# Kernel tuning notes

Measured on AMD Instinct MI355X. Metric: run time of the kernel, lower is better.

The kernel has to match this reference:

```python
import jax, jax.numpy as jnp
import numpy as np

B, C, H, W = 4, 64, 64, 64

def setup_inputs() -> dict:
    key = jax.random.key(0)
    ks = jax.random.split(key, 7)
    s = 1.0 / np.sqrt(C)
    return {
        "x": jax.random.normal(ks[0], (B, C, H, W), dtype=jnp.float32),
        "Wq": jax.random.normal(ks[1], (C, C), dtype=jnp.float32) * s,
        "bq": jax.random.normal(ks[2], (C,), dtype=jnp.float32) * s,
        "Wk": jax.random.normal(ks[3], (C, C), dtype=jnp.float32) * s,
        "bk": jax.random.normal(ks[4], (C,), dtype=jnp.float32) * s,
        "Wv": jax.random.normal(ks[5], (C, C), dtype=jnp.float32) * s,
        "bv": jax.random.normal(ks[6], (C,), dtype=jnp.float32) * s,
    }

def reference(x, Wq, bq, Wk, bk, Wv, bv):
    b, c, h, w = x.shape
    n = h * w
    xf = x.reshape(b, c, n)                                   # (B,C,N)
    # 1x1 convs == per-pixel linear maps over channels
    q = jnp.einsum('oc,bcn->bon', Wq, xf) + bq[None, :, None]  # (B,C,N)
    k = jnp.einsum('oc,bcn->bon', Wk, xf) + bk[None, :, None]  # (B,C,N)
    v = jnp.einsum('oc,bcn->bon', Wv, xf) + bv[None, :, None]  # (B,C,N)
    # energy = Q^T K : (B,N,N); note: no 1/sqrt(C) scaling in the original
    energy = jnp.einsum('bcn,bcm->bnm', q, k)
    attention = jax.nn.softmax(energy, axis=-1)
    # out = V @ attention^T : out[:, :, i] = sum_j V[:, :, j] * attention[i, j]
    out = jnp.einsum('bcm,bnm->bcn', v, attention)
    return out.reshape(b, c, h, w)
```

## Files before the change

### kernel.cpp

```cpp
#include <hip/hip_runtime.h>
#include <math.h>

#define T_N 4096
#define T_C 64
#define T_B 4
#define NSLICE 8
#define TILES_PER_SLICE (64 / NSLICE)

typedef __attribute__((ext_vector_type(8))) _Float16 f16x8;
typedef __attribute__((ext_vector_type(4))) _Float16 f16x4;
typedef __attribute__((ext_vector_type(4))) float f32x4;

__device__ inline unsigned short f2h(float f) {
    union { _Float16 h; unsigned short s; } u; u.h = (_Float16)f; return u.s;
}
__device__ inline float h2f(unsigned short s) {
    union { unsigned short s; _Float16 h; } u; u.s = s; return (float)u.h;
}

__global__ __launch_bounds__(256) void qkv_kernel(
    const float* __restrict__ x,
    const float* __restrict__ Wq, const float* __restrict__ bq,
    const float* __restrict__ Wk, const float* __restrict__ bk,
    const float* __restrict__ Wv, const float* __restrict__ bv,
    unsigned short* __restrict__ qt, unsigned short* __restrict__ kt,
    unsigned short* __restrict__ vb)
{
    __shared__ __align__(16) unsigned short xsh[32 * 72];
    __shared__ __align__(16) unsigned short xsl[32 * 72];
    __shared__ __align__(16) unsigned short wf[3][64 * 72];

    const int tid = threadIdx.x;
    const int n0  = blockIdx.x * 32;
    const int b   = blockIdx.y;
    const float* xb = x + (size_t)b * T_C * T_N;

    const float* Ws[3] = {Wq, Wk, Wv};
    #pragma unroll
    for (int p = 0; p < 3; ++p) {
        for (int i = tid; i < 1024; i += 256) {
            const int o = i >> 4, c4 = (i & 15) * 4;
            const float4 w4 = ((const float4*)Ws[p])[i];
            f16x4 wh;
            wh[0] = (_Float16)w4.x; wh[1] = (_Float16)w4.y;
            wh[2] = (_Float16)w4.z; wh[3] = (_Float16)w4.w;
            *(f16x4*)&wf[p][o * 72 + c4] = wh;
        }
    }
    for (int i = tid; i < 512; i += 256) {
        const int c = i >> 3, nj4 = (i & 7) * 4;
        const float4 xv = *(const float4*)&xb[c * T_N + n0 + nj4];
        const float xa[4] = {xv.x, xv.y, xv.z, xv.w};
        #pragma unroll
        for (int j = 0; j < 4; ++j) {
            const unsigned short h = f2h(xa[j]);
            xsh[(nj4 + j) * 72 + c] = h;
            xsl[(nj4 + j) * 72 + c] = f2h(xa[j] - h2f(h));
        }
    }
    __syncthreads();

    const int wv_  = tid >> 6;
    const int lane = tid & 63;
    const int quad = lane >> 4;
    const int col  = lane & 15;
    const int pst  = (wv_ & 1) * 16;
    const int oh   = (wv_ >> 1) * 2;
    const size_t bN = (size_t)b * T_N;

    f16x8 xh[2], xl[2];
    #pragma unroll
    for (int s = 0; s < 2; ++s) {
        xh[s] = *(const f16x8*)&xsh[(pst + col) * 72 + s * 32 + quad * 8];
        xl[s] = *(const f16x8*)&xsl[(pst + col) * 72 + s * 32 + quad * 8];
    }
    __syncthreads();

    const float* biases[3] = {bq, bk, bv};
    for (int p = 0; p < 3; ++p) {
        #pragma unroll
        for (int oo = 0; oo < 2; ++oo) {
            const int osub = oh + oo;
            f32x4 acc = (f32x4){0.f, 0.f, 0.f, 0.f};
            #pragma unroll
            for (int s = 0; s < 2; ++s) {
                const f16x8 wfr =
                    *(const f16x8*)&wf[p][(osub * 16 + col) * 72 + s * 32 + quad * 8];
                acc = __builtin_amdgcn_mfma_f32_16x16x32_f16(xh[s], wfr, acc, 0, 0, 0);
                acc = __builtin_amdgcn_mfma_f32_16x16x32_f16(xl[s], wfr, acc, 0, 0, 0);
            }
            const float bb = biases[p][osub * 16 + col];
            if (p < 2) {
                #pragma unroll
                for (int r = 0; r < 4; ++r)
                    xsh[(pst + quad * 4 + r) * 72 + osub * 16 + col] = f2h(acc[r] + bb);
            } else {
                union { ushort4 v; unsigned short s[4]; } hv;
                #pragma unroll
                for (int r = 0; r < 4; ++r) hv.s[r] = f2h(acc[r] + bb);
                *(ushort4*)&xsh[(osub * 16 + col) * 36 + pst + quad * 4] = hv.v;
            }
        }
        __syncthreads();
        if (p < 2) {
            const int pix = tid >> 3, c8 = (tid & 7) * 8;
            unsigned short* dst = (p == 0) ? qt : kt;
            *(f16x8*)&dst[(bN + n0 + pix) * 64 + c8] = *(const f16x8*)&xsh[pix * 72 + c8];
            __syncthreads();
        } else {
            const int o = tid >> 2, p8 = (tid & 3) * 8;
            *(f16x8*)&vb[((size_t)(b * 64 + o)) * T_N + n0 + p8] =
                *(const f16x8*)&xsh[o * 36 + p8];
        }
    }
}

__global__ __launch_bounds__(256, 4) void attn_kernel(
    const unsigned short* __restrict__ qt,
    const unsigned short* __restrict__ kt, const unsigned short* __restrict__ vb,
    unsigned short* __restrict__ o_part, float* __restrict__ mp, float* __restrict__ lp)
{
    __shared__ __align__(16) unsigned short ks[64 * 64];
    __shared__ __align__(16) unsigned short vs[64 * 64];

    const int tid   = threadIdx.x;
    const int n0    = blockIdx.x * 128;
    const int slice = blockIdx.y;
    const int b     = blockIdx.z;
    const int wv_   = tid >> 6;
    const int lane  = tid & 63;
    const int quad  = lane >> 4;
    const int col   = lane & 15;

    const size_t bN = (size_t)b * T_N;
    const int q0 = n0 + wv_ * 32 + col;
    const int q1 = q0 + 16;

    f16x8 qh0[2], qh1[2];
    #pragma unroll
    for (int s = 0; s < 2; ++s) {
        qh0[s] = *(const f16x8*)&qt[(bN + q0) * 64 + s * 32 + quad * 8];
        qh1[s] = *(const f16x8*)&qt[(bN + q1) * 64 + s * 32 + quad * 8];
    }

    const int row = tid >> 3, cc = tid & 7;
    const int pc  = (cc ^ (row & 7)) * 8;

    const int mbase = slice * TILES_PER_SLICE * 64;
    float4 p0, p1, p2, p3;
    p0 = *(const float4*)&kt[(bN + mbase + row) * 64 + cc * 8];
    p1 = *(const float4*)&kt[(bN + mbase + 32 + row) * 64 + cc * 8];
    p2 = *(const float4*)&vb[((size_t)(b * 64 + row)) * T_N + mbase + cc * 8];
    p3 = *(const float4*)&vb[((size_t)(b * 64 + 32 + row)) * T_N + mbase + cc * 8];

    f32x4 O0[4], O1[4];
    #pragma unroll
    for (int t = 0; t < 4; ++t) {
        O0[t] = (f32x4){0.f, 0.f, 0.f, 0.f};
        O1[t] = (f32x4){0.f, 0.f, 0.f, 0.f};
    }
    float m_st0 = -INFINITY, l_st0 = 0.f;
    float m_st1 = -INFINITY, l_st1 = 0.f;

    for (int it = 0; it < TILES_PER_SLICE; ++it) {
        __syncthreads();
        *(float4*)&ks[row * 64 + pc]        = p0;
        *(float4*)&ks[(32 + row) * 64 + pc] = p1;
        *(float4*)&vs[row * 64 + pc]        = p2;
        *(float4*)&vs[(32 + row) * 64 + pc] = p3;
        __syncthreads();

        {
            const int itn = (it + 1 < TILES_PER_SLICE) ? it + 1 : it;
            const int m0n = mbase + itn * 64;
            p0 = *(const float4*)&kt[(bN + m0n + row) * 64 + cc * 8];
            p1 = *(const float4*)&kt[(bN + m0n + 32 + row) * 64 + cc * 8];
            p2 = *(const float4*)&vb[((size_t)(b * 64 + row)) * T_N + m0n + cc * 8];
            p3 = *(const float4*)&vb[((size_t)(b * 64 + 32 + row)) * T_N + m0n + cc * 8];
        }

        f32x4 acc0[4], acc1[4];
        #pragma unroll
        for (int t = 0; t < 4; ++t) {
            acc0[t] = (f32x4){0.f, 0.f, 0.f, 0.f};
            acc1[t] = (f32x4){0.f, 0.f, 0.f, 0.f};
        }
        #pragma unroll
        for (int s = 0; s < 2; ++s) {
            #pragma unroll
            for (int t = 0; t < 4; ++t) {
                const f16x8 kf = *(const f16x8*)
                    &ks[(t * 16 + col) * 64 + (((s * 4 + quad) ^ (col & 7)) * 8)];
                acc0[t] = __builtin_amdgcn_mfma_f32_16x16x32_f16(kf, qh0[s], acc0[t], 0, 0, 0);
                acc1[t] = __builtin_amdgcn_mfma_f32_16x16x32_f16(kf, qh1[s], acc1[t], 0, 0, 0);
            }
        }

        f16x4 pf0[4], pf1[4];
        float alpha0, alpha1;
        {
            float mx = -INFINITY;
            #pragma unroll
            for (int t = 0; t < 4; ++t)
                #pragma unroll
                for (int r = 0; r < 4; ++r) mx = fmaxf(mx, acc0[t][r]);
            mx = fmaxf(mx, __shfl_xor(mx, 16));
            mx = fmaxf(mx, __shfl_xor(mx, 32));
            const float mnew = fmaxf(m_st0, mx);
            alpha0 = __expf(m_st0 - mnew);
            float sum = 0.f;
            #pragma unroll
            for (int t = 0; t < 4; ++t) {
                #pragma unroll
                for (int r = 0; r < 4; ++r) {
                    const float pv = __expf(acc0[t][r] - mnew);
                    sum += pv;
                    pf0[t][r] = (_Float16)pv;
                }
            }
            sum += __shfl_xor(sum, 16);
            sum += __shfl_xor(sum, 32);
            l_st0 = alpha0 * l_st0 + sum;
            m_st0 = mnew;
        }
        {
            float mx = -INFINITY;
            #pragma unroll
            for (int t = 0; t < 4; ++t)
                #pragma unroll
                for (int r = 0; r < 4; ++r) mx = fmaxf(mx, acc1[t][r]);
            mx = fmaxf(mx, __shfl_xor(mx, 16));
            mx = fmaxf(mx, __shfl_xor(mx, 32));
            const float mnew = fmaxf(m_st1, mx);
            alpha1 = __expf(m_st1 - mnew);
            float sum = 0.f;
            #pragma unroll
            for (int t = 0; t < 4; ++t) {
                #pragma unroll
                for (int r = 0; r < 4; ++r) {
                    const float pv = __expf(acc1[t][r] - mnew);
                    sum += pv;
                    pf1[t][r] = (_Float16)pv;
                }
            }
            sum += __shfl_xor(sum, 16);
            sum += __shfl_xor(sum, 32);
            l_st1 = alpha1 * l_st1 + sum;
            m_st1 = mnew;
        }

        #pragma unroll
        for (int tc = 0; tc < 4; ++tc) {
            O0[tc] *= alpha0;
            O1[tc] *= alpha1;
            #pragma unroll
            for (int t = 0; t < 4; ++t) {
                const f16x4 vf = *(const f16x4*)
                    &vs[(tc * 16 + col) * 64 +
                        (((2 * t + (quad >> 1)) ^ (col & 7)) * 8) + (quad & 1) * 4];
                O0[tc] = __builtin_amdgcn_mfma_f32_16x16x16f16(vf, pf0[t], O0[tc], 0, 0, 0);
                O1[tc] = __builtin_amdgcn_mfma_f32_16x16x16f16(vf, pf1[t], O1[tc], 0, 0, 0);
            }
        }
    }

    const size_t srow = (size_t)(slice * T_B + b) * 64;
    #pragma unroll
    for (int tc = 0; tc < 4; ++tc) {
        #pragma unroll
        for (int r = 0; r < 4; ++r) {
            const size_t crow = (srow + tc * 16 + quad * 4 + r) * T_N;
            o_part[crow + q0] = f2h(O0[tc][r]);
            o_part[crow + q1] = f2h(O1[tc][r]);
        }
    }
    if (quad == 0) {
        const size_t off = (size_t)(slice * T_B + b) * T_N;
        mp[off + q0] = m_st0;
        lp[off + q0] = l_st0;
        mp[off + q1] = m_st1;
        lp[off + q1] = l_st1;
    }
}

__global__ __launch_bounds__(256) void combine_kernel(
    const unsigned short* __restrict__ o_part,
    const float* __restrict__ mp, const float* __restrict__ lp,
    float* __restrict__ out)
{
    __shared__ float wn[NSLICE][32];

    const int tid = threadIdx.x;
    const int n0  = blockIdx.x * 32;
    const int b   = blockIdx.y;

    if (tid < 32) {
        float m_s[NSLICE], l_s[NSLICE];
        #pragma unroll
        for (int s = 0; s < NSLICE; ++s) {
            const size_t off = (size_t)(s * T_B + b) * T_N + n0 + tid;
            m_s[s] = mp[off];
            l_s[s] = lp[off];
        }
        float M = m_s[0];
        #pragma unroll
        for (int s = 1; s < NSLICE; ++s) M = fmaxf(M, m_s[s]);
        float w_s[NSLICE], L = 0.f;
        #pragma unroll
        for (int s = 0; s < NSLICE; ++s) {
            w_s[s] = __expf(m_s[s] - M);
            L += l_s[s] * w_s[s];
        }
        const float inv = 1.f / L;
        #pragma unroll
        for (int s = 0; s < NSLICE; ++s) wn[s][tid] = w_s[s] * inv;
    }
    __syncthreads();

    for (int t = tid; t < 512; t += 256) {
        const int c = t >> 3, g = t & 7;
        float4 acc = make_float4(0.f, 0.f, 0.f, 0.f);
        #pragma unroll
        for (int s = 0; s < NSLICE; ++s) {
            const ushort4 o4 = *(const ushort4*)
                &o_part[((size_t)((s * T_B + b) * 64 + c)) * T_N + n0 + g * 4];
            acc.x = fmaf(h2f(o4.x), wn[s][g * 4 + 0], acc.x);
            acc.y = fmaf(h2f(o4.y), wn[s][g * 4 + 1], acc.y);
            acc.z = fmaf(h2f(o4.z), wn[s][g * 4 + 2], acc.z);
            acc.w = fmaf(h2f(o4.w), wn[s][g * 4 + 3], acc.w);
        }
        *(float4*)&out[((size_t)(b * 64 + c)) * T_N + n0 + g * 4] = acc;
    }
}

extern "C" void kernel_launch(void* const* d_in, const int* in_sizes, int n_in,
                              void* d_out, int out_size, void* d_ws, size_t ws_size,
                              hipStream_t stream) {
    const float* x  = (const float*)d_in[0];
    const float* Wq = (const float*)d_in[1];
    const float* bq = (const float*)d_in[2];
    const float* Wk = (const float*)d_in[3];
    const float* bk = (const float*)d_in[4];
    const float* Wv = (const float*)d_in[5];
    const float* bv = (const float*)d_in[6];
    float* outp = (float*)d_out;

    const size_t elems = (size_t)T_B * T_N * T_C;
    unsigned short* qtp    = (unsigned short*)d_ws;
    unsigned short* ktp    = qtp + elems;
    unsigned short* vbuf   = ktp + elems;
    unsigned short* o_part = vbuf + elems;
    float* mp = (float*)(o_part + (size_t)NSLICE * elems);
    float* lp = mp + (size_t)NSLICE * T_B * T_N;

    qkv_kernel<<<dim3(T_N / 32, T_B), 256, 0, stream>>>(
        x, Wq, bq, Wk, bk, Wv, bv, qtp, ktp, vbuf);
    attn_kernel<<<dim3(T_N / 128, NSLICE, T_B), 256, 0, stream>>>(
        qtp, ktp, vbuf, o_part, mp, lp);
    combine_kernel<<<dim3(T_N / 32, T_B), 256, 0, stream>>>(
        o_part, mp, lp, outp);
}
```

Before: 112.3 us.

## Double-buffer K/V tiles with direct global-to-LDS loads and lazily rescale softmax

The attention kernel now streams K and V tiles straight into double-buffered LDS with global_load_lds. This drops the register staging copy and one barrier per tile. Wq and bq are prescaled by log2(e) so the softmax can use the native exp2 instruction. The running max and O rescale are skipped while the new tile max stays within 8 of the stored max. MFMA sections are wrapped in s_setprio to favor matrix issue. The changes double LDS use, which may lower occupancy, and they rely on the compiler inserting correct waits for the asynchronous LDS loads.

```diff
diff --git a/kernel.cpp b/kernel.cpp
--- a/kernel.cpp
+++ b/kernel.cpp
@@ -6,6 +6,7 @@
 #define T_B 4
 #define NSLICE 8
 #define TILES_PER_SLICE (64 / NSLICE)
+#define LOG2E 1.44269504088896f
 
 typedef __attribute__((ext_vector_type(8))) _Float16 f16x8;
 typedef __attribute__((ext_vector_type(4))) _Float16 f16x4;
@@ -17,6 +18,11 @@
 __device__ inline float h2f(unsigned short s) {
     union { unsigned short s; _Float16 h; } u; u.s = s; return (float)u.h;
 }
+__device__ inline float fexp2(float x) { return __builtin_amdgcn_exp2f(x); }
+
+#define DMA16(g, l) __builtin_amdgcn_global_load_lds(                         \
+    (const __attribute__((address_space(1))) void*)(g),                       \
+    (__attribute__((address_space(3))) void*)(l), 16, 0, 0)
 
 __global__ __launch_bounds__(256) void qkv_kernel(
     const float* __restrict__ x,
@@ -38,12 +44,13 @@
     const float* Ws[3] = {Wq, Wk, Wv};
     #pragma unroll
     for (int p = 0; p < 3; ++p) {
+        const float sc = (p == 0) ? LOG2E : 1.0f;
         for (int i = tid; i < 1024; i += 256) {
             const int o = i >> 4, c4 = (i & 15) * 4;
             const float4 w4 = ((const float4*)Ws[p])[i];
             f16x4 wh;
-            wh[0] = (_Float16)w4.x; wh[1] = (_Float16)w4.y;
-            wh[2] = (_Float16)w4.z; wh[3] = (_Float16)w4.w;
+            wh[0] = (_Float16)(w4.x * sc); wh[1] = (_Float16)(w4.y * sc);
+            wh[2] = (_Float16)(w4.z * sc); wh[3] = (_Float16)(w4.w * sc);
             *(f16x4*)&wf[p][o * 72 + c4] = wh;
         }
     }
@@ -89,7 +96,7 @@
                 acc = __builtin_amdgcn_mfma_f32_16x16x32_f16(xh[s], wfr, acc, 0, 0, 0);
                 acc = __builtin_amdgcn_mfma_f32_16x16x32_f16(xl[s], wfr, acc, 0, 0, 0);
             }
-            const float bb = biases[p][osub * 16 + col];
+            const float bb = biases[p][osub * 16 + col] * ((p == 0) ? LOG2E : 1.0f);
             if (p < 2) {
                 #pragma unroll
                 for (int r = 0; r < 4; ++r)
@@ -120,8 +127,8 @@
     const unsigned short* __restrict__ kt, const unsigned short* __restrict__ vb,
     unsigned short* __restrict__ o_part, float* __restrict__ mp, float* __restrict__ lp)
 {
-    __shared__ __align__(16) unsigned short ks[64 * 64];
-    __shared__ __align__(16) unsigned short vs[64 * 64];
+    __shared__ __align__(16) unsigned short ks[2][64 * 64];
+    __shared__ __align__(16) unsigned short vs[2][64 * 64];
 
     const int tid   = threadIdx.x;
     const int n0    = blockIdx.x * 128;
@@ -143,15 +150,20 @@
         qh1[s] = *(const f16x8*)&qt[(bN + q1) * 64 + s * 32 + quad * 8];
     }
 
-    const int row = tid >> 3, cc = tid & 7;
-    const int pc  = (cc ^ (row & 7)) * 8;
+    const int row  = tid >> 3, cc = tid & 7;
+    const int scc8 = (cc ^ (row & 7)) * 8;
+    const int ldst = row * 64 + cc * 8;
 
     const int mbase = slice * TILES_PER_SLICE * 64;
-    float4 p0, p1, p2, p3;
-    p0 = *(const float4*)&kt[(bN + mbase + row) * 64 + cc * 8];
-    p1 = *(const float4*)&kt[(bN + mbase + 32 + row) * 64 + cc * 8];
-    p2 = *(const float4*)&vb[((size_t)(b * 64 + row)) * T_N + mbase + cc * 8];
-    p3 = *(const float4*)&vb[((size_t)(b * 64 + 32 + row)) * T_N + mbase + cc * 8];
+    const unsigned short* kg = &kt[(bN + mbase + row) * 64 + scc8];
+    const unsigned short* vg = &vb[((size_t)(b * 64 + row)) * T_N + mbase + scc8];
+
+    DMA16(kg,                    &ks[0][ldst]);
+    DMA16(kg + 32 * 64,          &ks[0][32 * 64 + ldst]);
+    DMA16(vg,                    &vs[0][ldst]);
+    DMA16(vg + (size_t)32 * T_N, &vs[0][32 * 64 + ldst]);
+    kg += 64 * 64;
+    vg += 64;
 
     f32x4 O0[4], O1[4];
     #pragma unroll
@@ -164,20 +176,18 @@
 
     for (int it = 0; it < TILES_PER_SLICE; ++it) {
         __syncthreads();
-        *(float4*)&ks[row * 64 + pc]        = p0;
-        *(float4*)&ks[(32 + row) * 64 + pc] = p1;
-        *(float4*)&vs[row * 64 + pc]        = p2;
-        *(float4*)&vs[(32 + row) * 64 + pc] = p3;
-        __syncthreads();
-
-        {
-            const int itn = (it + 1 < TILES_PER_SLICE) ? it + 1 : it;
-            const int m0n = mbase + itn * 64;
-            p0 = *(const float4*)&kt[(bN + m0n + row) * 64 + cc * 8];
-            p1 = *(const float4*)&kt[(bN + m0n + 32 + row) * 64 + cc * 8];
-            p2 = *(const float4*)&vb[((size_t)(b * 64 + row)) * T_N + m0n + cc * 8];
-            p3 = *(const float4*)&vb[((size_t)(b * 64 + 32 + row)) * T_N + m0n + cc * 8];
-        }
+        const int cur = it & 1;
+        if (it + 1 < TILES_PER_SLICE) {
+            const int nb = cur ^ 1;
+            DMA16(kg,                    &ks[nb][ldst]);
+            DMA16(kg + 32 * 64,          &ks[nb][32 * 64 + ldst]);
+            DMA16(vg,                    &vs[nb][ldst]);
+            DMA16(vg + (size_t)32 * T_N, &vs[nb][32 * 64 + ldst]);
+            kg += 64 * 64;
+            vg += 64;
+        }
+        const unsigned short* ksb = ks[cur];
+        const unsigned short* vsb = vs[cur];
 
         f32x4 acc0[4], acc1[4];
         #pragma unroll
@@ -185,19 +195,20 @@
             acc0[t] = (f32x4){0.f, 0.f, 0.f, 0.f};
             acc1[t] = (f32x4){0.f, 0.f, 0.f, 0.f};
         }
+        __builtin_amdgcn_s_setprio(1);
         #pragma unroll
         for (int s = 0; s < 2; ++s) {
             #pragma unroll
             for (int t = 0; t < 4; ++t) {
                 const f16x8 kf = *(const f16x8*)
-                    &ks[(t * 16 + col) * 64 + (((s * 4 + quad) ^ (col & 7)) * 8)];
+                    &ksb[(t * 16 + col) * 64 + (((s * 4 + quad) ^ (col & 7)) * 8)];
                 acc0[t] = __builtin_amdgcn_mfma_f32_16x16x32_f16(kf, qh0[s], acc0[t], 0, 0, 0);
                 acc1[t] = __builtin_amdgcn_mfma_f32_16x16x32_f16(kf, qh1[s], acc1[t], 0, 0, 0);
             }
         }
+        __builtin_amdgcn_s_setprio(0);
 
         f16x4 pf0[4], pf1[4];
-        float alpha0, alpha1;
         {
             float mx = -INFINITY;
             #pragma unroll
@@ -206,22 +217,38 @@
                 for (int r = 0; r < 4; ++r) mx = fmaxf(mx, acc0[t][r]);
             mx = fmaxf(mx, __shfl_xor(mx, 16));
             mx = fmaxf(mx, __shfl_xor(mx, 32));
-            const float mnew = fmaxf(m_st0, mx);
-            alpha0 = __expf(m_st0 - mnew);
-            float sum = 0.f;
-            #pragma unroll
-            for (int t = 0; t < 4; ++t) {
-                #pragma unroll
-                for (int r = 0; r < 4; ++r) {
-                    const float pv = __expf(acc0[t][r] - mnew);
-                    sum += pv;
-                    pf0[t][r] = (_Float16)pv;
-                }
-            }
-            sum += __shfl_xor(sum, 16);
-            sum += __shfl_xor(sum, 32);
-            l_st0 = alpha0 * l_st0 + sum;
-            m_st0 = mnew;
+            if (__all(mx - m_st0 <= 8.f)) {
+                float sum = 0.f;
+                #pragma unroll
+                for (int t = 0; t < 4; ++t)
+                    #pragma unroll
+                    for (int r = 0; r < 4; ++r) {
+                        const float pv = fexp2(acc0[t][r] - m_st0);
+                        sum += pv;
+                        pf0[t][r] = (_Float16)pv;
+                    }
+                sum += __shfl_xor(sum, 16);
+                sum += __shfl_xor(sum, 32);
+                l_st0 += sum;
+            } else {
+                const float mnew  = fmaxf(m_st0, mx);
+                const float alpha = fexp2(m_st0 - mnew);
+                float sum = 0.f;
+                #pragma unroll
+                for (int t = 0; t < 4; ++t)
+                    #pragma unroll
+                    for (int r = 0; r < 4; ++r) {
+                        const float pv = fexp2(acc0[t][r] - mnew);
+                        sum += pv;
+                        pf0[t][r] = (_Float16)pv;
+                    }
+                sum += __shfl_xor(sum, 16);
+                sum += __shfl_xor(sum, 32);
+                l_st0 = alpha * l_st0 + sum;
+                m_st0 = mnew;
+                #pragma unroll
+                for (int tc = 0; tc < 4; ++tc) O0[tc] *= alpha;
+            }
         }
         {
             float mx = -INFINITY;
@@ -231,37 +258,53 @@
                 for (int r = 0; r < 4; ++r) mx = fmaxf(mx, acc1[t][r]);
             mx = fmaxf(mx, __shfl_xor(mx, 16));
             mx = fmaxf(mx, __shfl_xor(mx, 32));
-            const float mnew = fmaxf(m_st1, mx);
-            alpha1 = __expf(m_st1 - mnew);
-            float sum = 0.f;
-            #pragma unroll
-            for (int t = 0; t < 4; ++t) {
-                #pragma unroll
-                for (int r = 0; r < 4; ++r) {
-                    const float pv = __expf(acc1[t][r] - mnew);
-                    sum += pv;
-                    pf1[t][r] = (_Float16)pv;
-                }
-            }
-            sum += __shfl_xor(sum, 16);
-            sum += __shfl_xor(sum, 32);
-            l_st1 = alpha1 * l_st1 + sum;
-            m_st1 = mnew;
-        }
-
+            if (__all(mx - m_st1 <= 8.f)) {
+                float sum = 0.f;
+                #pragma unroll
+                for (int t = 0; t < 4; ++t)
+                    #pragma unroll
+                    for (int r = 0; r < 4; ++r) {
+                        const float pv = fexp2(acc1[t][r] - m_st1);
+                        sum += pv;
+                        pf1[t][r] = (_Float16)pv;
+                    }
+                sum += __shfl_xor(sum, 16);
+                sum += __shfl_xor(sum, 32);
+                l_st1 += sum;
+            } else {
+                const float mnew  = fmaxf(m_st1, mx);
+                const float alpha = fexp2(m_st1 - mnew);
+                float sum = 0.f;
+                #pragma unroll
+                for (int t = 0; t < 4; ++t)
+                    #pragma unroll
+                    for (int r = 0; r < 4; ++r) {
+                        const float pv = fexp2(acc1[t][r] - mnew);
+                        sum += pv;
+                        pf1[t][r] = (_Float16)pv;
+                    }
+                sum += __shfl_xor(sum, 16);
+                sum += __shfl_xor(sum, 32);
+                l_st1 = alpha * l_st1 + sum;
+                m_st1 = mnew;
+                #pragma unroll
+                for (int tc = 0; tc < 4; ++tc) O1[tc] *= alpha;
+            }
+        }
+
+        __builtin_amdgcn_s_setprio(1);
         #pragma unroll
         for (int tc = 0; tc < 4; ++tc) {
-            O0[tc] *= alpha0;
-            O1[tc] *= alpha1;
             #pragma unroll
             for (int t = 0; t < 4; ++t) {
                 const f16x4 vf = *(const f16x4*)
-                    &vs[(tc * 16 + col) * 64 +
-                        (((2 * t + (quad >> 1)) ^ (col & 7)) * 8) + (quad & 1) * 4];
+                    &vsb[(tc * 16 + col) * 64 +
+                         (((2 * t + (quad >> 1)) ^ (col & 7)) * 8) + (quad & 1) * 4];
                 O0[tc] = __builtin_amdgcn_mfma_f32_16x16x16f16(vf, pf0[t], O0[tc], 0, 0, 0);
                 O1[tc] = __builtin_amdgcn_mfma_f32_16x16x16f16(vf, pf1[t], O1[tc], 0, 0, 0);
             }
         }
+        __builtin_amdgcn_s_setprio(0);
     }
 
     const size_t srow = (size_t)(slice * T_B + b) * 64;
@@ -308,7 +351,7 @@
         float w_s[NSLICE], L = 0.f;
         #pragma unroll
         for (int s = 0; s < NSLICE; ++s) {
-            w_s[s] = __expf(m_s[s] - M);
+            w_s[s] = fexp2(m_s[s] - M);
             L += l_s[s] * w_s[s];
         }
         const float inv = 1.f / L;
```

After: 122.2 us. +8.9%, slower.

## Double-buffer K/V tiles via direct global-to-LDS loads and use exp2 softmax

Applied to the files above, without the earlier changes.

Replaces register-staged K/V tile loads with double-buffered global_load_lds copies straight into shared memory. The next tile is issued while the current one is computed, which removes a barrier and the register round trip per iteration. LOG2E is folded into the Q weights and bias so the softmax can use native exp2 instead of __expf. MFMA sections are also wrapped in s_setprio to favour matrix issue. The change relies on the barrier to wait for the asynchronous LDS writes and doubles LDS use, which may lower occupancy.

```diff
diff --git a/kernel.cpp b/kernel.cpp
--- a/kernel.cpp
+++ b/kernel.cpp
@@ -6,6 +6,7 @@
 #define T_B 4
 #define NSLICE 8
 #define TILES_PER_SLICE (64 / NSLICE)
+#define LOG2E 1.44269504088896f
 
 typedef __attribute__((ext_vector_type(8))) _Float16 f16x8;
 typedef __attribute__((ext_vector_type(4))) _Float16 f16x4;
@@ -17,6 +18,11 @@
 __device__ inline float h2f(unsigned short s) {
     union { unsigned short s; _Float16 h; } u; u.s = s; return (float)u.h;
 }
+__device__ inline float fexp2(float x) { return __builtin_amdgcn_exp2f(x); }
+
+#define DMA16(g, l) __builtin_amdgcn_global_load_lds(                         \
+    (const __attribute__((address_space(1))) void*)(g),                       \
+    (__attribute__((address_space(3))) void*)(l), 16, 0, 0)
 
 __global__ __launch_bounds__(256) void qkv_kernel(
     const float* __restrict__ x,
@@ -38,12 +44,13 @@
     const float* Ws[3] = {Wq, Wk, Wv};
     #pragma unroll
     for (int p = 0; p < 3; ++p) {
+        const float sc = (p == 0) ? LOG2E : 1.0f;
         for (int i = tid; i < 1024; i += 256) {
             const int o = i >> 4, c4 = (i & 15) * 4;
             const float4 w4 = ((const float4*)Ws[p])[i];
             f16x4 wh;
-            wh[0] = (_Float16)w4.x; wh[1] = (_Float16)w4.y;
-            wh[2] = (_Float16)w4.z; wh[3] = (_Float16)w4.w;
+            wh[0] = (_Float16)(w4.x * sc); wh[1] = (_Float16)(w4.y * sc);
+            wh[2] = (_Float16)(w4.z * sc); wh[3] = (_Float16)(w4.w * sc);
             *(f16x4*)&wf[p][o * 72 + c4] = wh;
         }
     }
@@ -89,7 +96,7 @@
                 acc = __builtin_amdgcn_mfma_f32_16x16x32_f16(xh[s], wfr, acc, 0, 0, 0);
                 acc = __builtin_amdgcn_mfma_f32_16x16x32_f16(xl[s], wfr, acc, 0, 0, 0);
             }
-            const float bb = biases[p][osub * 16 + col];
+            const float bb = biases[p][osub * 16 + col] * ((p == 0) ? LOG2E : 1.0f);
             if (p < 2) {
                 #pragma unroll
                 for (int r = 0; r < 4; ++r)
@@ -120,8 +127,8 @@
     const unsigned short* __restrict__ kt, const unsigned short* __restrict__ vb,
     unsigned short* __restrict__ o_part, float* __restrict__ mp, float* __restrict__ lp)
 {
-    __shared__ __align__(16) unsigned short ks[64 * 64];
-    __shared__ __align__(16) unsigned short vs[64 * 64];
+    __shared__ __align__(16) unsigned short ks[2][64 * 64];
+    __shared__ __align__(16) unsigned short vs[2][64 * 64];
 
     const int tid   = threadIdx.x;
     const int n0    = blockIdx.x * 128;
@@ -143,15 +150,18 @@
         qh1[s] = *(const f16x8*)&qt[(bN + q1) * 64 + s * 32 + quad * 8];
     }
 
-    const int row = tid >> 3, cc = tid & 7;
-    const int pc  = (cc ^ (row & 7)) * 8;
+    const int row  = tid >> 3, cc = tid & 7;
+    const int scc8 = (cc ^ (row & 7)) * 8;
+    const int ldst = row * 64 + cc * 8;
 
     const int mbase = slice * TILES_PER_SLICE * 64;
-    float4 p0, p1, p2, p3;
-    p0 = *(const float4*)&kt[(bN + mbase + row) * 64 + cc * 8];
-    p1 = *(const float4*)&kt[(bN + mbase + 32 + row) * 64 + cc * 8];
-    p2 = *(const float4*)&vb[((size_t)(b * 64 + row)) * T_N + mbase + cc * 8];
-    p3 = *(const float4*)&vb[((size_t)(b * 64 + 32 + row)) * T_N + mbase + cc * 8];
+    const unsigned short* kg_base = &kt[(bN + mbase + row) * 64 + scc8];
+    const unsigned short* vg_base = &vb[((size_t)(b * 64 + row)) * T_N + mbase + scc8];
+
+    DMA16(kg_base,                    &ks[0][ldst]);
+    DMA16(kg_base + 32 * 64,          &ks[0][32 * 64 + ldst]);
+    DMA16(vg_base,                    &vs[0][ldst]);
+    DMA16(vg_base + (size_t)32 * T_N, &vs[0][32 * 64 + ldst]);
 
     f32x4 O0[4], O1[4];
     #pragma unroll
@@ -164,20 +174,20 @@
 
     for (int it = 0; it < TILES_PER_SLICE; ++it) {
         __syncthreads();
-        *(float4*)&ks[row * 64 + pc]        = p0;
-        *(float4*)&ks[(32 + row) * 64 + pc] = p1;
-        *(float4*)&vs[row * 64 + pc]        = p2;
-        *(float4*)&vs[(32 + row) * 64 + pc] = p3;
-        __syncthreads();
+        const int cur = it & 1;
 
         {
-            const int itn = (it + 1 < TILES_PER_SLICE) ? it + 1 : it;
-            const int m0n = mbase + itn * 64;
-            p0 = *(const float4*)&kt[(bN + m0n + row) * 64 + cc * 8];
-            p1 = *(const float4*)&kt[(bN + m0n + 32 + row) * 64 + cc * 8];
-            p2 = *(const float4*)&vb[((size_t)(b * 64 + row)) * T_N + m0n + cc * 8];
-            p3 = *(const float4*)&vb[((size_t)(b * 64 + 32 + row)) * T_N + m0n + cc * 8];
-        }
+            const int itn = (it < TILES_PER_SLICE - 1) ? it + 1 : it;
+            const unsigned short* kgn = kg_base + itn * (64 * 64);
+            const unsigned short* vgn = vg_base + itn * 64;
+            const int nb = cur ^ 1;
+            DMA16(kgn,                    &ks[nb][ldst]);
+            DMA16(kgn + 32 * 64,          &ks[nb][32 * 64 + ldst]);
+            DMA16(vgn,                    &vs[nb][ldst]);
+            DMA16(vgn + (size_t)32 * T_N, &vs[nb][32 * 64 + ldst]);
+        }
+        const unsigned short* ksb = ks[cur];
+        const unsigned short* vsb = vs[cur];
 
         f32x4 acc0[4], acc1[4];
         #pragma unroll
@@ -185,16 +195,18 @@
             acc0[t] = (f32x4){0.f, 0.f, 0.f, 0.f};
             acc1[t] = (f32x4){0.f, 0.f, 0.f, 0.f};
         }
+        __builtin_amdgcn_s_setprio(1);
         #pragma unroll
         for (int s = 0; s < 2; ++s) {
             #pragma unroll
             for (int t = 0; t < 4; ++t) {
                 const f16x8 kf = *(const f16x8*)
-                    &ks[(t * 16 + col) * 64 + (((s * 4 + quad) ^ (col & 7)) * 8)];
+                    &ksb[(t * 16 + col) * 64 + (((s * 4 + quad) ^ (col & 7)) * 8)];
                 acc0[t] = __builtin_amdgcn_mfma_f32_16x16x32_f16(kf, qh0[s], acc0[t], 0, 0, 0);
                 acc1[t] = __builtin_amdgcn_mfma_f32_16x16x32_f16(kf, qh1[s], acc1[t], 0, 0, 0);
             }
         }
+        __builtin_amdgcn_s_setprio(0);
 
         f16x4 pf0[4], pf1[4];
         float alpha0, alpha1;
@@ -207,13 +219,13 @@
             mx = fmaxf(mx, __shfl_xor(mx, 16));
             mx = fmaxf(mx, __shfl_xor(mx, 32));
             const float mnew = fmaxf(m_st0, mx);
-            alpha0 = __expf(m_st0 - mnew);
+            alpha0 = fexp2(m_st0 - mnew);
             float sum = 0.f;
             #pragma unroll
             for (int t = 0; t < 4; ++t) {
                 #pragma unroll
                 for (int r = 0; r < 4; ++r) {
-                    const float pv = __expf(acc0[t][r] - mnew);
+                    const float pv = fexp2(acc0[t][r] - mnew);
                     sum += pv;
                     pf0[t][r] = (_Float16)pv;
                 }
@@ -232,13 +244,13 @@
             mx = fmaxf(mx, __shfl_xor(mx, 16));
             mx = fmaxf(mx, __shfl_xor(mx, 32));
             const float mnew = fmaxf(m_st1, mx);
-            alpha1 = __expf(m_st1 - mnew);
+            alpha1 = fexp2(m_st1 - mnew);
             float sum = 0.f;
             #pragma unroll
             for (int t = 0; t < 4; ++t) {
                 #pragma unroll
                 for (int r = 0; r < 4; ++r) {
-                    const float pv = __expf(acc1[t][r] - mnew);
+                    const float pv = fexp2(acc1[t][r] - mnew);
                     sum += pv;
                     pf1[t][r] = (_Float16)pv;
                 }
@@ -249,6 +261,7 @@
             m_st1 = mnew;
         }
 
+        __builtin_amdgcn_s_setprio(1);
         #pragma unroll
         for (int tc = 0; tc < 4; ++tc) {
             O0[tc] *= alpha0;
@@ -256,12 +269,13 @@
             #pragma unroll
             for (int t = 0; t < 4; ++t) {
                 const f16x4 vf = *(const f16x4*)
-                    &vs[(tc * 16 + col) * 64 +
-                        (((2 * t + (quad >> 1)) ^ (col & 7)) * 8) + (quad & 1) * 4];
+                    &vsb[(tc * 16 + col) * 64 +
+                         (((2 * t + (quad >> 1)) ^ (col & 7)) * 8) + (quad & 1) * 4];
                 O0[tc] = __builtin_amdgcn_mfma_f32_16x16x16f16(vf, pf0[t], O0[tc], 0, 0, 0);
                 O1[tc] = __builtin_amdgcn_mfma_f32_16x16x16f16(vf, pf1[t], O1[tc], 0, 0, 0);
             }
         }
+        __builtin_amdgcn_s_setprio(0);
     }
 
     const size_t srow = (size_t)(slice * T_B + b) * 64;
@@ -308,7 +322,7 @@
         float w_s[NSLICE], L = 0.f;
         #pragma unroll
         for (int s = 0; s < NSLICE; ++s) {
-            w_s[s] = __expf(m_s[s] - M);
+            w_s[s] = fexp2(m_s[s] - M);
             L += l_s[s] * w_s[s];
         }
         const float inv = 1.f / L;
```

Result: slower. 115.5 us (+2.9%).
